# Optimization experiments

Measured on AMD Instinct MI355X. Metric: run time of the kernel, lower is better.

## Reference

```python
import jax, jax.numpy as jnp
import numpy as np

N = 50000          # nodes
E = 640000         # edges (before self-loops)
DIM_FEATS = 128
DIM_H = 32
HEADS1 = 8
NUM_CLASS = 16
NEG_SLOPE_ATT = 0.2   # PyG GATv2Conv default negative_slope
NEG_SLOPE_OUT = 0.01  # F.leaky_relu default


def setup_inputs() -> dict:
    key = jax.random.key(0)
    ks = jax.random.split(key, 12)
    s = 0.1
    x = jax.random.normal(ks[0], (N, DIM_FEATS), dtype=jnp.float32)
    edge_index = jax.random.randint(ks[1], (2, E), 0, N, dtype=jnp.int32)
    # GATv2Conv layer 1: dim_feats -> dim_h per head, 8 heads, concat
    W1l = jax.random.normal(ks[2], (DIM_FEATS, HEADS1 * DIM_H), dtype=jnp.float32) * s
    W1r = jax.random.normal(ks[3], (DIM_FEATS, HEADS1 * DIM_H), dtype=jnp.float32) * s
    att1 = jax.random.normal(ks[4], (HEADS1, DIM_H), dtype=jnp.float32) * s
    b1 = jnp.zeros((HEADS1 * DIM_H,), dtype=jnp.float32)
    # GATv2Conv layer 2: 256 -> num_class, 1 head, concat=False
    W2l = jax.random.normal(ks[5], (HEADS1 * DIM_H, NUM_CLASS), dtype=jnp.float32) * s
    W2r = jax.random.normal(ks[6], (HEADS1 * DIM_H, NUM_CLASS), dtype=jnp.float32) * s
    att2 = jax.random.normal(ks[7], (1, NUM_CLASS), dtype=jnp.float32) * s
    b2 = jnp.zeros((NUM_CLASS,), dtype=jnp.float32)
    return {"x": x, "edge_index": edge_index, "W1l": W1l, "W1r": W1r,
            "att1": att1, "b1": b1, "W2l": W2l, "W2r": W2r,
            "att2": att2, "b2": b2}


def _segment_softmax(scores, seg, num_segments):
    # scores: [E, H], seg: [E] destination node ids
    m = jax.ops.segment_max(scores, seg, num_segments=num_segments)  # [N, H]
    e = jnp.exp(scores - m[seg])
    denom = jax.ops.segment_sum(e, seg, num_segments=num_segments)   # [N, H]
    return e / (denom[seg] + 1e-16)


def _gatv2_layer(x, src, dst, Wl, Wr, att, bias, heads, out_ch, concat):
    n = x.shape[0]
    xl = (x @ Wl).reshape(n, heads, out_ch)  # source transform
    xr = (x @ Wr).reshape(n, heads, out_ch)  # target transform
    # per-edge GATv2 score: a^T LeakyReLU(xl[j] + xr[i])
    e = jax.nn.leaky_relu(xl[src] + xr[dst], negative_slope=NEG_SLOPE_ATT)  # [E,H,F]
    alpha = jnp.einsum('ehf,hf->eh', e, att)                                # [E,H]
    alpha = _segment_softmax(alpha, dst, n)
    msg = xl[src] * alpha[:, :, None]                                       # [E,H,F]
    out = jax.ops.segment_sum(msg, dst, num_segments=n)                     # [N,H,F]
    out = out.reshape(n, heads * out_ch) if concat else out.mean(axis=1)
    return out + bias


def reference(x, edge_index, W1l, W1r, att1, b1, W2l, W2r, att2, b2):
    # add_self_loops=True (PyG GATv2Conv default)
    loop = jnp.arange(N, dtype=edge_index.dtype)
    src = jnp.concatenate([edge_index[0], loop])
    dst = jnp.concatenate([edge_index[1], loop])
    # eval mode: all dropouts are identity
    h = _gatv2_layer(x, src, dst, W1l, W1r, att1, b1, HEADS1, DIM_H, concat=True)
    h = jax.nn.elu(h)
    h = _gatv2_layer(h, src, dst, W2l, W2r, att2, b2, 1, NUM_CLASS, concat=False)
    return jax.nn.leaky_relu(h, negative_slope=NEG_SLOPE_OUT)
```

## Files before the change

kernel.cpp:

```cpp
#include <hip/hip_runtime.h>
#include <math.h>

#define NN 50000
#define E0 640000
#define ET 690000
#define F1 128
#define D1 256
#define C2 16
#define NB 196
#define MPAD 50048
#define PADK 136
#define LOG2E 1.4426950408889634f
#define NBK1 782

typedef _Float16 f16x8 __attribute__((ext_vector_type(8)));
typedef _Float16 h2 __attribute__((ext_vector_type(2)));
typedef __attribute__((ext_vector_type(4))) float f32x4;

__device__ __forceinline__ unsigned short f2h(float f) {
  union { _Float16 h; unsigned short u; } c;
  c.h = (_Float16)f;
  return c.u;
}
__device__ __forceinline__ float h2f(unsigned short u) {
  union { unsigned short u; _Float16 h; } c; c.u = u; return (float)c.h;
}
__device__ __forceinline__ h2 u2h2(unsigned u) {
  union { unsigned u; h2 h; } c; c.u = u; return c.h;
}
__device__ __forceinline__ unsigned h22u(h2 h) {
  union { h2 h; unsigned u; } c; c.h = h; return c.u;
}

__global__ __launch_bounds__(256) void k_prep(
    const float* __restrict__ Wl, const float* __restrict__ Wr,
    const float* __restrict__ W2l, const float* __restrict__ W2r,
    const int* __restrict__ ei,
    unsigned short* __restrict__ wt, unsigned short* __restrict__ wt2,
    int* __restrict__ deg) {
  const int b = blockIdx.x;
  if (b < 256) {
    int tid = b * 256 + threadIdx.x;
    int n = tid >> 7, k = tid & 127;
    float v = (n < 256) ? Wl[k * 256 + n] : Wr[k * 256 + (n - 256)];
    wt[tid] = f2h(v);
  } else if (b < 288) {
    int tid = (b - 256) * 256 + threadIdx.x;
    int n = tid >> 8, k = tid & 255;
    float v = (n < 16) ? W2l[k * 16 + n] : W2r[k * 16 + (n - 16)];
    wt2[tid] = f2h(v);
  } else {
    int e = (b - 288) * 256 + threadIdx.x;
    if (e >= ET) return;
    int d = (e < E0) ? ei[E0 + e] : (e - E0);
    atomicAdd(&deg[d], 1);
  }
}

__global__ __launch_bounds__(256) void k_gemm1m(
    const float* __restrict__ x, const unsigned short* __restrict__ wt,
    unsigned short* __restrict__ xlh, unsigned short* __restrict__ xrh) {
  __shared__ unsigned short Al[128 * PADK];
  __shared__ unsigned short Bl[128 * PADK];
  const int t = threadIdx.x;
  const int m0 = blockIdx.x * 128;
  const int n0 = blockIdx.y * 128;
  {
    const int r = t >> 4;
    const int c = (t & 15) * 8;
#pragma unroll
    for (int p = 0; p < 8; ++p) {
      const int row = r + p * 16;
      const int rg = m0 + row;
      const float* xp = &x[(size_t)(rg < NN ? rg : NN - 1) * F1 + c];
      float4 lo = *(const float4*)xp;
      float4 hi = *(const float4*)(xp + 4);
      h2 q0 = h2{(_Float16)lo.x, (_Float16)lo.y};
      h2 q1 = h2{(_Float16)lo.z, (_Float16)lo.w};
      h2 q2 = h2{(_Float16)hi.x, (_Float16)hi.y};
      h2 q3 = h2{(_Float16)hi.z, (_Float16)hi.w};
      uint4 st; st.x = h22u(q0); st.y = h22u(q1); st.z = h22u(q2); st.w = h22u(q3);
      *(uint4*)&Al[row * PADK + c] = st;
      *(float4*)&Bl[row * PADK + c] = *(const float4*)&wt[(size_t)(n0 + row) * F1 + c];
    }
  }
  __syncthreads();
  const int wave = t >> 6, lane = t & 63;
  const int mw = (wave >> 1) * 64, nw = (wave & 1) * 64;
  const int fr = lane & 15, fq = lane >> 4;
  f32x4 acc[4][4] = {};
#pragma unroll
  for (int ks = 0; ks < 4; ++ks) {
    const int ko = ks * 32 + fq * 8;
    f16x8 a[4], b[4];
#pragma unroll
    for (int i = 0; i < 4; ++i)
      a[i] = *(const f16x8*)&Al[(mw + i * 16 + fr) * PADK + ko];
#pragma unroll
    for (int j = 0; j < 4; ++j)
      b[j] = *(const f16x8*)&Bl[(nw + j * 16 + fr) * PADK + ko];
#pragma unroll
    for (int i = 0; i < 4; ++i)
#pragma unroll
      for (int j = 0; j < 4; ++j)
        acc[i][j] = __builtin_amdgcn_mfma_f32_16x16x32_f16(a[i], b[j], acc[i][j], 0, 0, 0);
  }
  unsigned short* outp = (n0 < 256) ? xlh : xrh;
  const int cb = (n0 & 255) + nw + fr;
#pragma unroll
  for (int j = 0; j < 4; ++j) {
    const int col = cb + j * 16;
    const int head = col >> 5, f = col & 31;
    unsigned short* hp = outp + (size_t)head * NN * 32 + f;
#pragma unroll
    for (int i = 0; i < 4; ++i) {
      const int gm0 = m0 + mw + i * 16 + fq * 4;
#pragma unroll
      for (int r = 0; r < 4; ++r) {
        const int gm = gm0 + r;
        if (gm < NN) hp[(size_t)gm * 32] = f2h(acc[i][j][r]);
      }
    }
  }
}

__global__ __launch_bounds__(256) void k_scan_part(const int* __restrict__ deg,
                                                   int* __restrict__ part) {
  int i = blockIdx.x * 256 + threadIdx.x;
  int v = (i < NN) ? deg[i] : 0;
  v += __shfl_xor(v, 1);  v += __shfl_xor(v, 2);  v += __shfl_xor(v, 4);
  v += __shfl_xor(v, 8);  v += __shfl_xor(v, 16); v += __shfl_xor(v, 32);
  __shared__ int w[4];
  if ((threadIdx.x & 63) == 0) w[threadIdx.x >> 6] = v;
  __syncthreads();
  if (threadIdx.x == 0) part[blockIdx.x] = w[0] + w[1] + w[2] + w[3];
}

__global__ __launch_bounds__(256) void k_scan_apply(int* __restrict__ deg,
                                                    const int* __restrict__ part,
                                                    int* __restrict__ offs) {
  __shared__ int lds[256];
  __shared__ int red[4];
  const int b = blockIdx.x, t = threadIdx.x;
  const int i = b * 256 + t;
  int v = (i < NN) ? deg[i] : 0;
  lds[t] = v;
  int pp = 0;
  for (int j = t; j < b; j += 256) pp += part[j];
  pp += __shfl_xor(pp, 1);  pp += __shfl_xor(pp, 2);  pp += __shfl_xor(pp, 4);
  pp += __shfl_xor(pp, 8);  pp += __shfl_xor(pp, 16); pp += __shfl_xor(pp, 32);
  if ((t & 63) == 0) red[t >> 6] = pp;
  __syncthreads();
  const int prefix = red[0] + red[1] + red[2] + red[3];
  for (int off = 1; off < 256; off <<= 1) {
    int u = (t >= off) ? lds[t - off] : 0;
    __syncthreads();
    lds[t] += u;
    __syncthreads();
  }
  int excl = prefix + lds[t] - v;
  if (i < NN) { offs[i] = excl; deg[i] = excl; }
  if (b == NB - 1 && t == 255) offs[NN] = prefix + lds[255];
}

__global__ void k_scatter(const int* __restrict__ ei, int* __restrict__ cur,
                          unsigned short* __restrict__ csr) {
  int e = blockIdx.x * 256 + threadIdx.x;
  if (e >= ET) return;
  int s, d;
  if (e < E0) { s = ei[e]; d = ei[E0 + e]; } else { s = d = e - E0; }
  int pos = atomicAdd(&cur[d], 1);
  csr[pos] = (unsigned short)s;
}

__global__ __launch_bounds__(256) void k_agg1(
    const unsigned short* __restrict__ xlh, const unsigned short* __restrict__ xrh,
    unsigned short* __restrict__ hb,
    const int* __restrict__ offs, const unsigned short* __restrict__ csr,
    const float* __restrict__ att, const float* __restrict__ b1) {
  const int b = blockIdx.x;
  const int head = b & 7;
  const int wave = threadIdx.x >> 6;
  const int lane = threadIdx.x & 63;
  const int g = lane >> 2;
  const int j4 = lane & 3;
  const int n = (b >> 3) * 64 + wave * 16 + g;
  const bool valid = n < NN;
  const int colh = j4 * 8;
  const int col = head * 32 + colh;
  const unsigned short* xlhead = xlh + (size_t)head * NN * 32;

  const int nc = valid ? n : 0;
  const uint4 xru = *(const uint4*)&xrh[((size_t)head * NN + nc) * 32 + colh];
  h2 xr2[4];
  xr2[0] = u2h2(xru.x); xr2[1] = u2h2(xru.y);
  xr2[2] = u2h2(xru.z); xr2[3] = u2h2(xru.w);
  float at8[8];
  *(float4*)&at8[0] = *(const float4*)&att[col];
  *(float4*)&at8[4] = *(const float4*)&att[col + 4];
  h2 ath6[4], ath4[4];
#pragma unroll
  for (int j = 0; j < 4; ++j) {
    ath6[j] = h2{(_Float16)(at8[2 * j] * (0.6f * LOG2E)),
                 (_Float16)(at8[2 * j + 1] * (0.6f * LOG2E))};
    ath4[j] = h2{(_Float16)(at8[2 * j] * (0.4f * LOG2E)),
                 (_Float16)(at8[2 * j + 1] * (0.4f * LOG2E))};
  }
  float l = 0.f;
  h2 acc2[4] = {h2{0, 0}, h2{0, 0}, h2{0, 0}, h2{0, 0}};
  const int beg = valid ? offs[n] : 0;
  const int fin = valid ? offs[n + 1] : 0;

  auto score = [&](const h2* xh) -> float {
    float cv = 0.f, ca = 0.f;
#pragma unroll
    for (int j = 0; j < 4; ++j) {
      h2 v = xh[j] + xr2[j];
      h2 a = u2h2(h22u(v) & 0x7FFF7FFFu);
      cv = __builtin_amdgcn_fdot2(v, ath6[j], cv, false);
      ca = __builtin_amdgcn_fdot2(a, ath4[j], ca, false);
    }
    float c = cv + ca;
    c += __shfl_xor(c, 1);
    c += __shfl_xor(c, 2);
    return c;
  };

  int idx = beg;
  for (; idx + 1 < fin; idx += 2) {
    const int s0 = csr[idx], s1 = csr[idx + 1];
    const uint4 w0 = *(const uint4*)&xlhead[(size_t)s0 * 32 + colh];
    const uint4 w1 = *(const uint4*)&xlhead[(size_t)s1 * 32 + colh];
    h2 xh0[4], xh1[4];
    xh0[0] = u2h2(w0.x); xh0[1] = u2h2(w0.y); xh0[2] = u2h2(w0.z); xh0[3] = u2h2(w0.w);
    xh1[0] = u2h2(w1.x); xh1[1] = u2h2(w1.y); xh1[2] = u2h2(w1.z); xh1[3] = u2h2(w1.w);
    const float c0 = score(xh0);
    const float c1 = score(xh1);
    const float p0 = exp2f(c0), p1 = exp2f(c1);
    l += p0 + p1;
    const _Float16 p0h = (_Float16)p0, p1h = (_Float16)p1;
    const h2 p02 = h2{p0h, p0h}, p12 = h2{p1h, p1h};
#pragma unroll
    for (int j = 0; j < 4; ++j) acc2[j] += p02 * xh0[j] + p12 * xh1[j];
  }
  if (idx < fin) {
    const int s0 = csr[idx];
    const uint4 w0 = *(const uint4*)&xlhead[(size_t)s0 * 32 + colh];
    h2 xh0[4];
    xh0[0] = u2h2(w0.x); xh0[1] = u2h2(w0.y); xh0[2] = u2h2(w0.z); xh0[3] = u2h2(w0.w);
    const float c0 = score(xh0);
    const float p0 = exp2f(c0);
    l += p0;
    const _Float16 p0h = (_Float16)p0;
    const h2 p02 = h2{p0h, p0h};
#pragma unroll
    for (int j = 0; j < 4; ++j) acc2[j] += p02 * xh0[j];
  }
  if (valid) {
    const float rl = 1.f / (l + 1e-16f);
    float b8[8], o[8];
    *(float4*)&b8[0] = *(const float4*)&b1[col];
    *(float4*)&b8[4] = *(const float4*)&b1[col + 4];
#pragma unroll
    for (int j = 0; j < 4; ++j) {
      o[2 * j]     = (float)acc2[j][0] * rl + b8[2 * j];
      o[2 * j + 1] = (float)acc2[j][1] * rl + b8[2 * j + 1];
    }
#pragma unroll
    for (int k = 0; k < 8; ++k) o[k] = o[k] > 0.f ? o[k] : expm1f(o[k]);
    ushort4 p;
    p.x = f2h(o[0]); p.y = f2h(o[1]); p.z = f2h(o[2]); p.w = f2h(o[3]);
    ushort4 q;
    q.x = f2h(o[4]); q.y = f2h(o[5]); q.z = f2h(o[6]); q.w = f2h(o[7]);
    uint4 packed;
    packed.x = *(unsigned*)&p.x; packed.y = *(unsigned*)&p.z;
    packed.z = *(unsigned*)&q.x; packed.w = *(unsigned*)&q.z;
    *(uint4*)&hb[(size_t)n * D1 + col] = packed;
  }
}

__global__ __launch_bounds__(256) void k_gemm2m(
    const unsigned short* __restrict__ hb, const unsigned short* __restrict__ wt2,
    unsigned short* __restrict__ h2lh, float* __restrict__ h2r) {
  const int t = threadIdx.x;
  const int wave = t >> 6, lane = t & 63;
  const int fr = lane & 15, fq = lane >> 4;
  const int m0 = blockIdx.x * 128 + wave * 32;
  f32x4 acc[2][2] = {};
#pragma unroll
  for (int ks = 0; ks < 8; ++ks) {
    const int ko = ks * 32 + fq * 8;
    f16x8 a[2], b[2];
#pragma unroll
    for (int i = 0; i < 2; ++i) {
      int row = m0 + i * 16 + fr; if (row >= NN) row = NN - 1;
      a[i] = *(const f16x8*)&hb[(size_t)row * D1 + ko];
    }
#pragma unroll
    for (int j = 0; j < 2; ++j)
      b[j] = *(const f16x8*)&wt2[(j * 16 + fr) * 256 + ko];
#pragma unroll
    for (int i = 0; i < 2; ++i)
#pragma unroll
      for (int j = 0; j < 2; ++j)
        acc[i][j] = __builtin_amdgcn_mfma_f32_16x16x32_f16(a[i], b[j], acc[i][j], 0, 0, 0);
  }
#pragma unroll
  for (int i = 0; i < 2; ++i) {
    const int gm0 = m0 + i * 16 + fq * 4;
#pragma unroll
    for (int r = 0; r < 4; ++r) {
      const int gm = gm0 + r;
      if (gm < NN) {
        h2lh[(size_t)gm * C2 + fr] = f2h(acc[i][0][r]);
        h2r[(size_t)gm * C2 + fr] = acc[i][1][r];
      }
    }
  }
}

__global__ __launch_bounds__(256) void k_agg2(
    const unsigned short* __restrict__ h2lh, const float* __restrict__ h2r,
    const int* __restrict__ offs, const unsigned short* __restrict__ csr,
    const float* __restrict__ att2, const float* __restrict__ b2,
    float* __restrict__ out) {
  const int wave = threadIdx.x >> 6;
  const int lane = threadIdx.x & 63;
  const int n = blockIdx.x * 4 + wave;
  if (n >= NN) return;
  const int c = lane & 15, g = lane >> 4;
  const float xr_v = h2r[(size_t)n * C2 + c];
  const float att_v = att2[c] * LOG2E;
  float l = 0.f, acc = 0.f;
  const int beg = offs[n], fin = offs[n + 1];
  for (int idx = beg + g; idx < fin; idx += 4) {
    int s = csr[idx];
    float xlv = h2f(h2lh[(size_t)s * C2 + c]);
    float v = xlv + xr_v;
    v = fmaxf(v, 0.2f * v);
    float sc0 = v * att_v;
    sc0 += __shfl_xor(sc0, 1);
    sc0 += __shfl_xor(sc0, 2);
    sc0 += __shfl_xor(sc0, 4);
    sc0 += __shfl_xor(sc0, 8);
    float p = exp2f(sc0);
    l += p;
    acc = fmaf(p, xlv, acc);
  }
  l += __shfl_xor(l, 16);   l += __shfl_xor(l, 32);
  acc += __shfl_xor(acc, 16); acc += __shfl_xor(acc, 32);
  float o = acc / (l + 1e-16f) + b2[c];
  o = o > 0.f ? o : 0.01f * o;
  if (lane < 16) out[(size_t)n * C2 + c] = o;
}

extern "C" void kernel_launch(void* const* d_in, const int* in_sizes, int n_in,
                              void* d_out, int out_size, void* d_ws, size_t ws_size,
                              hipStream_t stream) {
  const float* x    = (const float*)d_in[0];
  const int*   ei   = (const int*)d_in[1];
  const float* W1l  = (const float*)d_in[2];
  const float* W1r  = (const float*)d_in[3];
  const float* att1 = (const float*)d_in[4];
  const float* b1   = (const float*)d_in[5];
  const float* W2l  = (const float*)d_in[6];
  const float* W2r  = (const float*)d_in[7];
  const float* att2 = (const float*)d_in[8];
  const float* b2   = (const float*)d_in[9];
  float* out = (float*)d_out;

  unsigned short* xlh = (unsigned short*)d_ws;
  unsigned short* xrh = xlh + (size_t)NN * D1;
  unsigned short* hb  = xrh + (size_t)NN * D1;
  int* deg  = (int*)(hb + (size_t)NN * D1);
  int* part = deg + NN;
  int* offs = part + NB;
  unsigned short* csr = (unsigned short*)(offs + NN + 1);
  unsigned short* wt  = csr + ET + 2;
  unsigned short* wt2 = wt + 512 * F1;
  unsigned short* h2lh = xlh;
  float* h2r = (float*)(h2lh + (size_t)NN * C2);

  hipMemsetAsync(deg, 0, NN * sizeof(int), stream);
  k_prep<<<288 + (ET + 255) / 256, 256, 0, stream>>>(
      W1l, W1r, W2l, W2r, ei, wt, wt2, deg);
  k_gemm1m<<<dim3(MPAD / 128, 4), 256, 0, stream>>>(x, wt, xlh, xrh);
  k_scan_part<<<NB, 256, 0, stream>>>(deg, part);
  k_scan_apply<<<NB, 256, 0, stream>>>(deg, part, offs);
  k_scatter<<<(ET + 255) / 256, 256, 0, stream>>>(ei, deg, csr);
  k_agg1<<<NBK1 * 8, 256, 0, stream>>>(xlh, xrh, hb, offs, csr, att1, b1);
  k_gemm2m<<<(NN + 127) / 128, 256, 0, stream>>>(hb, wt2, h2lh, h2r);
  k_agg2<<<NN / 4, 256, 0, stream>>>(h2lh, h2r, offs, csr, att2, b2, out);
}
```

Baseline: 271.6 us.

## Sort nodes by degree for agg1 load balance and use DPP reductions

Builds a 64-bucket degree histogram during the scan, prefix-sums it in the scatter kernel, and adds a permutation kernel that orders nodes by descending degree. k_agg1 then processes nodes in that order, so the 16 nodes sharing a wave have similar edge counts and less lane divergence. The small cross-lane reductions in agg1 and agg2 also switch from shuffles to DPP adds. The cost is an extra kernel launch, global atomics on the bucket counters, and scattered per-node reads and writes in agg1.

```diff
diff --git a/kernel.cpp b/kernel.cpp
--- a/kernel.cpp
+++ b/kernel.cpp
@@ -30,6 +30,12 @@
 }
 __device__ __forceinline__ unsigned h22u(h2 h) {
   union { h2 h; unsigned u; } c; c.h = h; return c.u;
+}
+
+template <int CTRL>
+__device__ __forceinline__ float dpp_add(float c) {
+  int t = __builtin_amdgcn_update_dpp(0, __builtin_bit_cast(int, c), CTRL, 0xF, 0xF, true);
+  return c + __builtin_bit_cast(float, t);
 }
 
 __global__ __launch_bounds__(256) void k_prep(
@@ -138,19 +144,26 @@
 
 __global__ __launch_bounds__(256) void k_scan_apply(int* __restrict__ deg,
                                                     const int* __restrict__ part,
-                                                    int* __restrict__ offs) {
+                                                    int* __restrict__ offs,
+                                                    int* __restrict__ bhist) {
   __shared__ int lds[256];
   __shared__ int red[4];
+  __shared__ int bh[64];
   const int b = blockIdx.x, t = threadIdx.x;
   const int i = b * 256 + t;
   int v = (i < NN) ? deg[i] : 0;
   lds[t] = v;
+  if (t < 64) bh[t] = 0;
   int pp = 0;
   for (int j = t; j < b; j += 256) pp += part[j];
   pp += __shfl_xor(pp, 1);  pp += __shfl_xor(pp, 2);  pp += __shfl_xor(pp, 4);
   pp += __shfl_xor(pp, 8);  pp += __shfl_xor(pp, 16); pp += __shfl_xor(pp, 32);
   if ((t & 63) == 0) red[t >> 6] = pp;
   __syncthreads();
+  if (i < NN) {
+    int bkt = 63 - (v < 63 ? v : 63);
+    atomicAdd(&bh[bkt], 1);
+  }
   const int prefix = red[0] + red[1] + red[2] + red[3];
   for (int off = 1; off < 256; off <<= 1) {
     int u = (t >= off) ? lds[t - off] : 0;
@@ -161,10 +174,22 @@
   int excl = prefix + lds[t] - v;
   if (i < NN) { offs[i] = excl; deg[i] = excl; }
   if (b == NB - 1 && t == 255) offs[NN] = prefix + lds[255];
+  if (t < 64 && bh[t] > 0) atomicAdd(&bhist[t], bh[t]);
 }
 
 __global__ void k_scatter(const int* __restrict__ ei, int* __restrict__ cur,
-                          unsigned short* __restrict__ csr) {
+                          unsigned short* __restrict__ csr,
+                          const int* __restrict__ bhist, int* __restrict__ bcur) {
+  if (blockIdx.x == 0 && threadIdx.x < 64) {
+    int t = threadIdx.x;
+    int v = bhist[t];
+    int s = v;
+    for (int off = 1; off < 64; off <<= 1) {
+      int u = __shfl_up(s, off);
+      if (t >= off) s += u;
+    }
+    bcur[t] = s - v;
+  }
   int e = blockIdx.x * 256 + threadIdx.x;
   if (e >= ET) return;
   int s, d;
@@ -173,25 +198,48 @@
   csr[pos] = (unsigned short)s;
 }
 
+__global__ __launch_bounds__(256) void k_perm(const int* __restrict__ offs,
+                                              int* __restrict__ bcur,
+                                              int* __restrict__ perm) {
+  __shared__ int lh[64];
+  __shared__ int lbase[64];
+  const int t = threadIdx.x;
+  const int i = blockIdx.x * 256 + t;
+  if (t < 64) lh[t] = 0;
+  __syncthreads();
+  int bkt = 0, lpos = 0;
+  const bool valid = i < NN;
+  if (valid) {
+    int d = offs[i + 1] - offs[i];
+    bkt = 63 - (d < 63 ? d : 63);
+    lpos = atomicAdd(&lh[bkt], 1);
+  }
+  __syncthreads();
+  if (t < 64 && lh[t] > 0) lbase[t] = atomicAdd(&bcur[t], lh[t]);
+  __syncthreads();
+  if (valid) perm[lbase[bkt] + lpos] = i;
+}
+
 __global__ __launch_bounds__(256) void k_agg1(
     const unsigned short* __restrict__ xlh, const unsigned short* __restrict__ xrh,
     unsigned short* __restrict__ hb,
     const int* __restrict__ offs, const unsigned short* __restrict__ csr,
-    const float* __restrict__ att, const float* __restrict__ b1) {
+    const float* __restrict__ att, const float* __restrict__ b1,
+    const int* __restrict__ perm) {
   const int b = blockIdx.x;
   const int head = b & 7;
   const int wave = threadIdx.x >> 6;
   const int lane = threadIdx.x & 63;
   const int g = lane >> 2;
   const int j4 = lane & 3;
-  const int n = (b >> 3) * 64 + wave * 16 + g;
-  const bool valid = n < NN;
+  const int idxn = (b >> 3) * 64 + wave * 16 + g;
+  const bool valid = idxn < NN;
+  const int n = valid ? perm[idxn] : 0;
   const int colh = j4 * 8;
   const int col = head * 32 + colh;
   const unsigned short* xlhead = xlh + (size_t)head * NN * 32;
 
-  const int nc = valid ? n : 0;
-  const uint4 xru = *(const uint4*)&xrh[((size_t)head * NN + nc) * 32 + colh];
+  const uint4 xru = *(const uint4*)&xrh[((size_t)head * NN + n) * 32 + colh];
   h2 xr2[4];
   xr2[0] = u2h2(xru.x); xr2[1] = u2h2(xru.y);
   xr2[2] = u2h2(xru.z); xr2[3] = u2h2(xru.w);
@@ -221,8 +269,8 @@
       ca = __builtin_amdgcn_fdot2(a, ath4[j], ca, false);
     }
     float c = cv + ca;
-    c += __shfl_xor(c, 1);
-    c += __shfl_xor(c, 2);
+    c = dpp_add<0xB1>(c);
+    c = dpp_add<0x4E>(c);
     return c;
   };
 
@@ -339,10 +387,10 @@
     float v = xlv + xr_v;
     v = fmaxf(v, 0.2f * v);
     float sc0 = v * att_v;
-    sc0 += __shfl_xor(sc0, 1);
-    sc0 += __shfl_xor(sc0, 2);
-    sc0 += __shfl_xor(sc0, 4);
-    sc0 += __shfl_xor(sc0, 8);
+    sc0 = dpp_add<0xB1>(sc0);
+    sc0 = dpp_add<0x4E>(sc0);
+    sc0 = dpp_add<0x124>(sc0);
+    sc0 = dpp_add<0x128>(sc0);
     float p = exp2f(sc0);
     l += p;
     acc = fmaf(p, xlv, acc);
@@ -373,22 +421,26 @@
   unsigned short* xrh = xlh + (size_t)NN * D1;
   unsigned short* hb  = xrh + (size_t)NN * D1;
   int* deg  = (int*)(hb + (size_t)NN * D1);
-  int* part = deg + NN;
+  int* bhist = deg + NN;
+  int* bcur  = bhist + 64;
+  int* part = bcur + 64;
   int* offs = part + NB;
-  unsigned short* csr = (unsigned short*)(offs + NN + 1);
+  int* perm = offs + NN + 1;
+  unsigned short* csr = (unsigned short*)(perm + NN);
   unsigned short* wt  = csr + ET + 2;
   unsigned short* wt2 = wt + 512 * F1;
   unsigned short* h2lh = xlh;
   float* h2r = (float*)(h2lh + (size_t)NN * C2);
 
-  hipMemsetAsync(deg, 0, NN * sizeof(int), stream);
+  hipMemsetAsync(deg, 0, (NN + 64) * sizeof(int), stream);
   k_prep<<<288 + (ET + 255) / 256, 256, 0, stream>>>(
       W1l, W1r, W2l, W2r, ei, wt, wt2, deg);
   k_gemm1m<<<dim3(MPAD / 128, 4), 256, 0, stream>>>(x, wt, xlh, xrh);
   k_scan_part<<<NB, 256, 0, stream>>>(deg, part);
-  k_scan_apply<<<NB, 256, 0, stream>>>(deg, part, offs);
-  k_scatter<<<(ET + 255) / 256, 256, 0, stream>>>(ei, deg, csr);
-  k_agg1<<<NBK1 * 8, 256, 0, stream>>>(xlh, xrh, hb, offs, csr, att1, b1);
+  k_scan_apply<<<NB, 256, 0, stream>>>(deg, part, offs, bhist);
+  k_scatter<<<(ET + 255) / 256, 256, 0, stream>>>(ei, deg, csr, bhist, bcur);
+  k_perm<<<NB, 256, 0, stream>>>(offs, bcur, perm);
+  k_agg1<<<NBK1 * 8, 256, 0, stream>>>(xlh, xrh, hb, offs, csr, att1, b1, perm);
   k_gemm2m<<<(NN + 127) / 128, 256, 0, stream>>>(hb, wt2, h2lh, h2r);
   k_agg2<<<NN / 4, 256, 0, stream>>>(h2lh, h2r, offs, csr, att2, b2, out);
 }
```

Measured after the change: 274.9 us. No clear change (+1.2%).
